# Kernel tuning notes

Measured on AMD Instinct MI355X. Metric: run time of the kernel, lower is better.

## Reference

```python
import jax, jax.numpy as jnp
import numpy as np

B, N, E = 64, 1024, 16384  # graphs, nodes per graph, edges per graph
N_ITER = 5
NORMALIZE = True
NUM_INIT_LABELS = 16


def _unique_inverse(h):
    """Equivalent of torch.unique(h, sorted=True, return_inverse=True)[1] for 1-D h."""
    order = jnp.argsort(h)
    sh = h[order]
    bnd = jnp.concatenate([jnp.zeros(1, jnp.int32), (sh[1:] != sh[:-1]).astype(jnp.int32)])
    ranks = jnp.cumsum(bnd)  # dense rank in sorted-unique order
    return jnp.zeros_like(ranks).at[order].set(ranks)


def _wl_iteration(mask, labels, hash_w):
    """One WL iteration for all graphs.
    mask: [B,N,N] bool dense adjacency (sparse-to-dense, as in the torch code)
    labels: [B,N] int32
    hash_w: [2] float32 (Linear(2,1,bias=False) weight)
    Returns new labels [B,N] int32.
    """
    w0, w1 = hash_w[0], hash_w[1]
    lab_f = labels.astype(jnp.float32)
    deg = mask.sum(-1).astype(jnp.float32)                      # [B,N] valid-neighbor count
    K = deg.max(axis=-1, keepdims=True)                         # per-graph max_neighbors
    # sum of neighbor labels (gather+reduce over the dense mask, memory-bound)
    seg = jnp.einsum('bij,bj->bi', mask.astype(jnp.float32), lab_f)  # [B,N]
    # torch builds [N,max_neighbors] rows: node label in col 0-feature, sorted
    # neighbor labels (padded with -1) in col 1-feature, hashes each pair with
    # w0*node + w1*neigh and sums over columns. Closed form (sort is sum-invariant):
    #   K*w0*node + w1*(sum_neighbors - (K - deg))
    hashed = K * w0 * lab_f + w1 * (seg + deg - K)              # [B,N]
    return jax.vmap(_unique_inverse)(hashed)


def setup_inputs() -> dict:
    key = jax.random.key(0)
    k1, k2, k3, k4 = jax.random.split(key, 4)
    edge_src = jax.random.randint(k1, (B, E), 0, N, dtype=jnp.int32)
    edge_dst = jax.random.randint(k2, (B, E), 0, N, dtype=jnp.int32)
    labels = jax.random.randint(k3, (B, N), 0, NUM_INIT_LABELS, dtype=jnp.int32)
    hash_w = jax.random.normal(k4, (2,), dtype=jnp.float32)
    return {"edge_src": edge_src, "edge_dst": edge_dst, "labels": labels, "hash_w": hash_w}


def reference(edge_src, edge_dst, labels, hash_w):
    # sparse-to-dense neighbor mask, as in the torch module
    b_idx = jnp.arange(B, dtype=jnp.int32)[:, None]
    mask = jnp.zeros((B, N, N), dtype=bool).at[b_idx, edge_src, edge_dst].set(True)

    all_labels = [labels]
    for _ in range(N_ITER):
        all_labels.append(_wl_iteration(mask, all_labels[-1], hash_w))

    # feature vectors: per graph, bincount of labels summed over all iterations.
    # Labels are always < N (unique-inverse ranks < N; initial labels < 16),
    # so N bins is a tight static upper bound for torch's max_label+1; the extra
    # zero columns do not change the Gram matrix.
    labels_all = jnp.stack(all_labels, axis=1).reshape(B, -1)   # [B, (n_iter+1)*N]
    feats = jax.vmap(lambda l: jnp.zeros((N,), jnp.float32).at[l].add(1.0))(labels_all)

    kernel = feats @ feats.T                                    # [B,B]
    if NORMALIZE:
        d = jnp.sqrt(jnp.diag(kernel))
        kernel = kernel / (d[None, :] * d[:, None])
    return kernel
```

## Files before the change

### kernel.cpp

```cpp
#include <hip/hip_runtime.h>

#define B 64
#define N 1024
#define E 16384
#define WPR 32
#define NITER 5
#define CSR_SLOTS (E + N)
#define MAXP 20

#define FEATS_OFF 0
#define DIAG_OFF  ((size_t)B * N * 4)

__global__ void __launch_bounds__(1024) wl_mega_k(const int* __restrict__ src,
                                                  const int* __restrict__ dstp,
                                                  const int* __restrict__ lab0,
                                                  const float* __restrict__ hw,
                                                  unsigned int* __restrict__ feats,
                                                  float* __restrict__ diag) {
    __shared__ union {
        unsigned int chunk[N * WPR];
        struct {
            unsigned short nbr[CSR_SLOTS];
            struct {
                int hist[N];
                int scan[N];
                float grp[N];
                int flag[N];
            } pb;
            int meta[N];
            unsigned short perm[N];
            int dh[256];
            int dtop[256];
        } s;
    } u;
    __shared__ int s_lab[N + 2];
    __shared__ unsigned int s_feats[N];
    __shared__ int s_wsum[16];
    __shared__ int s_kp[16];
    __shared__ float s_mn[16], s_mx[16];
    __shared__ float s_gmn, s_gmx;
    __shared__ int s_K;
    __shared__ int s_anytie;
    int b = blockIdx.x, t = threadIdx.x;
    int lane = t & 63, w = t >> 6;

#pragma unroll
    for (int k = 0; k < 8; ++k)
        ((uint4*)u.chunk)[t + k * 1024] = make_uint4(0, 0, 0, 0);
    int l0 = lab0[(size_t)b * N + t];
    s_lab[t] = l0;
    s_feats[t] = 0;
    if (t == 0) { s_lab[N] = 0; s_anytie = 0; }
    __syncthreads();
#pragma unroll
    for (int v = 0; v < 16; ++v) {
        unsigned long long m = __ballot(l0 == v);
        if (lane == v) {
            int c = __popcll(m);
            if (c) atomicAdd(&s_feats[v], (unsigned)c);
        }
    }

    const int* sg = src + (size_t)b * E;
    const int* dg_ = dstp + (size_t)b * E;
#pragma unroll
    for (int k = 0; k < 16; ++k) {
        int es = sg[t + k * 1024];
        int ed = dg_[t + k * 1024];
        int wlog = ed >> 5;
        int g = wlog >> 2;
        int p = (g + es) & 7;
        atomicOr(&u.chunk[es * WPR + p * 4 + (wlog & 3)], 1u << (ed & 31));
    }
    __syncthreads();
    uint4 r[8];
    {
        const uint4* row4 = (const uint4*)(u.chunk + t * WPR);
#pragma unroll
        for (int g = 0; g < 8; ++g)
            r[g] = row4[(g + t) & 7];
    }
    __syncthreads();

    int dg = 0;
#pragma unroll
    for (int k = 0; k < 8; ++k)
        dg += __popc(r[k].x) + __popc(r[k].y) + __popc(r[k].z) + __popc(r[k].w);
    int alloc = (dg + 1) & ~1;

    int f = alloc;
#pragma unroll
    for (int d2 = 1; d2 < 64; d2 <<= 1) {
        int v = __shfl_up(f, d2);
        if (lane >= d2) f += v;
    }
    int km = dg;
#pragma unroll
    for (int o = 32; o > 0; o >>= 1) km = max(km, __shfl_down(km, o));
    if (lane == 63) s_wsum[w] = f;
    if (lane == 0)  s_kp[w] = km;
    __syncthreads();
    if (w == 0) {
        int orig = (lane < 16) ? s_wsum[lane] : 0;
        int v = orig;
#pragma unroll
        for (int d2 = 1; d2 < 16; d2 <<= 1) {
            int uu = __shfl_up(v, d2);
            if (lane >= d2) v += uu;
        }
        if (lane < 16) s_wsum[lane] = v - orig;
        int kk = (lane < 16) ? s_kp[lane] : 0;
#pragma unroll
        for (int m2 = 8; m2 >= 1; m2 >>= 1) kk = max(kk, __shfl_xor(kk, m2));
        if (lane == 0) s_K = kk;
    }
    __syncthreads();
    int start = (f - alloc) + s_wsum[w];
    u.s.pb.hist[t] = 0;
    u.s.pb.flag[t] = 0;
    if (t < 256) u.s.dh[t] = 0;

    {
        int idx = start;
#pragma unroll
        for (int k = 0; k < 8; ++k) {
            unsigned int wv[4] = { r[k].x, r[k].y, r[k].z, r[k].w };
#pragma unroll
            for (int c2 = 0; c2 < 4; ++c2) {
                unsigned int word = wv[c2];
                int bb = (k * 4 + c2) << 5;
                while (word) {
                    int j = __ffs(word) - 1;
                    word &= word - 1;
                    u.s.nbr[idx++] = (unsigned short)(bb + j);
                }
            }
        }
        if (dg & 1) u.s.nbr[idx] = (unsigned short)N;
    }
    u.s.meta[t] = (start << 11) | dg;
    float Kf = (float)s_K;
    float w0 = hw[0], w1 = hw[1];
    __syncthreads();

    atomicAdd(&u.s.dh[min(dg, 255)], 1);
    __syncthreads();
    if (w == 0) {
        int h0 = u.s.dh[lane * 4], h1 = u.s.dh[lane * 4 + 1];
        int h2 = u.s.dh[lane * 4 + 2], h3 = u.s.dh[lane * 4 + 3];
        int c1 = h0 + h1, c2 = c1 + h2, c3 = c2 + h3;
        int ex = c3;
#pragma unroll
        for (int d2 = 1; d2 < 64; d2 <<= 1) {
            int v = __shfl_up(ex, d2);
            if (lane >= d2) ex += v;
        }
        ex -= c3;
        u.s.dtop[lane * 4]     = N - (ex + h0);
        u.s.dtop[lane * 4 + 1] = N - (ex + c1);
        u.s.dtop[lane * 4 + 2] = N - (ex + c2);
        u.s.dtop[lane * 4 + 3] = N - (ex + c3);
    }
    __syncthreads();
    {
        int pos = atomicAdd(&u.s.dtop[min(dg, 255)], 1);
        u.s.perm[pos] = (unsigned short)t;
    }
    __syncthreads();
    int v_node = u.s.perm[t];
    int mv = u.s.meta[v_node];
    int vdeg = mv & 2047;
    int vpstart = (mv >> 11) >> 1;
    int vpairs = ((vdeg + 1) & ~1) >> 1;
    int lab_reg = s_lab[v_node];
    const unsigned int* nbr32 = (const unsigned int*)u.s.nbr;
    unsigned int pw[MAXP];
#pragma unroll
    for (int k = 0; k < MAXP; ++k) {
        unsigned int pk = 0u;
        if (k < vpairs) pk = nbr32[vpstart + k];
        pw[k] = pk;
    }

    for (int it = 0; it < NITER; ++it) {
        int ssum = 0;
#pragma unroll
        for (int k = 0; k < MAXP; ++k) if (k < vpairs) {
            unsigned int pr = pw[k];
            ssum += s_lab[pr & 0xFFFFu] + s_lab[pr >> 16];
        }
        for (int k = MAXP; k < vpairs; ++k) {
            unsigned int pr = nbr32[vpstart + k];
            ssum += s_lab[pr & 0xFFFFu] + s_lab[pr >> 16];
        }
        float t1 = __fmul_rn(__fmul_rn(Kf, w0), (float)lab_reg);
        float t2 = __fmul_rn(w1, __fsub_rn(__fadd_rn((float)ssum, (float)vdeg), Kf));
        float h  = __fadd_rn(t1, t2);

        float mn = h, mx = h;
#pragma unroll
        for (int o = 32; o > 0; o >>= 1) {
            mn = fminf(mn, __shfl_down(mn, o));
            mx = fmaxf(mx, __shfl_down(mx, o));
        }
        if (lane == 0) { s_mn[w] = mn; s_mx[w] = mx; }
        __syncthreads();
        if (w == 0) {
            float a = (lane < 16) ? s_mn[lane] : 3.4e38f;
            float c = (lane < 16) ? s_mx[lane] : -3.4e38f;
#pragma unroll
            for (int m2 = 8; m2 >= 1; m2 >>= 1) {
                a = fminf(a, __shfl_xor(a, m2));
                c = fmaxf(c, __shfl_xor(c, m2));
            }
            if (lane == 0) { s_gmn = a; s_gmx = c; }
        }
        __syncthreads();
        float fmn = s_gmn;
        float span = s_gmx - fmn;
        float scale = (span > 0.f) ? (1023.0f / span) : 0.f;
        int bucket = min((int)((h - fmn) * scale), 1023);
        int off_in = atomicAdd(&u.s.pb.hist[bucket], 1);
        __syncthreads();

        f = u.s.pb.hist[t];
#pragma unroll
        for (int d2 = 1; d2 < 64; d2 <<= 1) {
            int v = __shfl_up(f, d2);
            if (lane >= d2) f += v;
        }
        if (lane == 63) s_wsum[w] = f;
        __syncthreads();
        if (w == 0) {
            int orig = (lane < 16) ? s_wsum[lane] : 0;
            int v = orig;
#pragma unroll
            for (int d2 = 1; d2 < 16; d2 <<= 1) {
                int uu = __shfl_up(v, d2);
                if (lane >= d2) v += uu;
            }
            if (lane < 16) s_wsum[lane] = v - orig;
        }
        __syncthreads();
        u.s.pb.scan[t] = f + s_wsum[w];
        __syncthreads();

        int bs = u.s.pb.scan[bucket] - u.s.pb.hist[bucket];
        int be = u.s.pb.scan[bucket];
        u.s.pb.grp[bs + off_in] = h;
        __syncthreads();

        int c = bs;
        int eq = 0;
        for (int k = bs; k < be; ++k) {
            float g = u.s.pb.grp[k];
            c += (g < h);
            eq += (g == h);
        }
        if (eq > 1) s_anytie = it + 1;
        u.s.pb.hist[t] = 0;
        __syncthreads();

        int rank;
        if (s_anytie != it + 1) {
            rank = c;
            s_lab[v_node] = rank;
            lab_reg = rank;
            s_feats[rank] += 1u;
        } else {
            u.s.pb.flag[c] = 1;
            __syncthreads();
            int f2 = u.s.pb.flag[t];
#pragma unroll
            for (int d2 = 1; d2 < 64; d2 <<= 1) {
                int v = __shfl_up(f2, d2);
                if (lane >= d2) f2 += v;
            }
            if (lane == 63) s_wsum[w] = f2;
            __syncthreads();
            if (w == 0) {
                int orig = (lane < 16) ? s_wsum[lane] : 0;
                int v = orig;
#pragma unroll
                for (int d2 = 1; d2 < 16; d2 <<= 1) {
                    int uu = __shfl_up(v, d2);
                    if (lane >= d2) v += uu;
                }
                if (lane < 16) s_wsum[lane] = v - orig;
            }
            __syncthreads();
            u.s.pb.scan[t] = f2 + s_wsum[w];
            u.s.pb.flag[t] = 0;
            __syncthreads();
            rank = u.s.pb.scan[c] - 1;
            s_lab[v_node] = rank;
            lab_reg = rank;
            atomicAdd(&s_feats[rank], 1u);
        }
        __syncthreads();
    }

    unsigned int fv = s_feats[t];
    feats[(size_t)b * N + t] = fv;
    int sq = (int)(fv * fv);
#pragma unroll
    for (int o = 32; o > 0; o >>= 1) sq += __shfl_down(sq, o);
    if (lane == 0) s_wsum[w] = sq;
    __syncthreads();
    if (t == 0) {
        int tot = 0;
#pragma unroll
        for (int k = 0; k < 16; ++k) tot += s_wsum[k];
        diag[b] = (float)tot;
    }
}

__global__ void __launch_bounds__(256) gram_k(const unsigned int* __restrict__ feats,
                                              const float* __restrict__ diag,
                                              float* __restrict__ out) {
    __shared__ unsigned int s_fi[N];
    int i = blockIdx.x, t = threadIdx.x;
    int lane = t & 63, w = t >> 6;
    ((uint4*)s_fi)[t] = ((const uint4*)(feats + (size_t)i * N))[t];
    __syncthreads();
    float di = diag[i];
    for (int jj = 0; jj < 16; ++jj) {
        int j = w * 16 + jj;
        const uint4* fj = (const uint4*)(feats + (size_t)j * N);
        const uint4* fi = (const uint4*)s_fi;
        int s = 0;
#pragma unroll
        for (int k = 0; k < 4; ++k) {
            uint4 vb = fj[lane + k * 64];
            uint4 va = fi[lane + k * 64];
            s += (int)(va.x * vb.x) + (int)(va.y * vb.y)
               + (int)(va.z * vb.z) + (int)(va.w * vb.w);
        }
#pragma unroll
        for (int off = 32; off > 0; off >>= 1) s += __shfl_down(s, off);
        if (lane == 0) out[i * B + j] = (float)s / sqrtf(di * diag[j]);
    }
}

extern "C" void kernel_launch(void* const* d_in, const int* in_sizes, int n_in,
                              void* d_out, int out_size, void* d_ws, size_t ws_size,
                              hipStream_t stream) {
    const int*   esrc = (const int*)d_in[0];
    const int*   edst = (const int*)d_in[1];
    const int*   lab0 = (const int*)d_in[2];
    const float* hw   = (const float*)d_in[3];

    char* ws = (char*)d_ws;
    unsigned int* feats = (unsigned int*)(ws + FEATS_OFF);
    float*        diag  = (float*)(ws + DIAG_OFF);

    wl_mega_k<<<B, 1024, 0, stream>>>(esrc, edst, lab0, hw, feats, diag);
    gram_k<<<B, 256, 0, stream>>>(feats, diag, (float*)d_out);
}
```

Baseline: 110.5 us.

## Drop block barriers via redundant per-wave reductions and defer fast-path histogram

Every wave now redundantly computes the cross-wave min/max, the scan offsets and the max degree from shared partials with xor shuffles. This replaces the wave-0 reduction plus an extra __syncthreads in setup and in each WL iteration. The edge and label global loads are hoisted to the top of the kernel so their latency overlaps shared-memory zeroing. In the tie-free path the ranks form a permutation, so each bin's count increment is replaced by a per-thread counter added once at the end. The cost is a few redundant shuffles and LDS reads per wave, plus more live registers for the preloaded edges.

```diff
diff --git a/kernel.cpp b/kernel.cpp
--- a/kernel.cpp
+++ b/kernel.cpp
@@ -38,16 +38,23 @@
     __shared__ int s_wsum[16];
     __shared__ int s_kp[16];
     __shared__ float s_mn[16], s_mx[16];
-    __shared__ float s_gmn, s_gmx;
-    __shared__ int s_K;
     __shared__ int s_anytie;
     int b = blockIdx.x, t = threadIdx.x;
     int lane = t & 63, w = t >> 6;
 
+    const int* sg = src + (size_t)b * E;
+    const int* dg_ = dstp + (size_t)b * E;
+    int es[16], ed[16];
+#pragma unroll
+    for (int k = 0; k < 16; ++k) {
+        es[k] = sg[t + k * 1024];
+        ed[k] = dg_[t + k * 1024];
+    }
+    int l0 = lab0[(size_t)b * N + t];
+    float w0 = hw[0], w1 = hw[1];
 #pragma unroll
     for (int k = 0; k < 8; ++k)
         ((uint4*)u.chunk)[t + k * 1024] = make_uint4(0, 0, 0, 0);
-    int l0 = lab0[(size_t)b * N + t];
     s_lab[t] = l0;
     s_feats[t] = 0;
     if (t == 0) { s_lab[N] = 0; s_anytie = 0; }
@@ -61,16 +68,12 @@
         }
     }
 
-    const int* sg = src + (size_t)b * E;
-    const int* dg_ = dstp + (size_t)b * E;
 #pragma unroll
     for (int k = 0; k < 16; ++k) {
-        int es = sg[t + k * 1024];
-        int ed = dg_[t + k * 1024];
-        int wlog = ed >> 5;
+        int wlog = ed[k] >> 5;
         int g = wlog >> 2;
-        int p = (g + es) & 7;
-        atomicOr(&u.chunk[es * WPR + p * 4 + (wlog & 3)], 1u << (ed & 31));
+        int p = (g + es[k]) & 7;
+        atomicOr(&u.chunk[es[k] * WPR + p * 4 + (wlog & 3)], 1u << (ed[k] & 31));
     }
     __syncthreads();
     uint4 r[8];
@@ -100,22 +103,18 @@
     if (lane == 63) s_wsum[w] = f;
     if (lane == 0)  s_kp[w] = km;
     __syncthreads();
-    if (w == 0) {
-        int orig = (lane < 16) ? s_wsum[lane] : 0;
-        int v = orig;
-#pragma unroll
-        for (int d2 = 1; d2 < 16; d2 <<= 1) {
-            int uu = __shfl_up(v, d2);
-            if (lane >= d2) v += uu;
-        }
-        if (lane < 16) s_wsum[lane] = v - orig;
-        int kk = (lane < 16) ? s_kp[lane] : 0;
+    float Kf;
+    int start;
+    {
+        int vv = ((lane & 15) < w) ? s_wsum[lane & 15] : 0;
+#pragma unroll
+        for (int m2 = 1; m2 < 16; m2 <<= 1) vv += __shfl_xor(vv, m2);
+        start = (f - alloc) + vv;
+        int kk = s_kp[lane & 15];
 #pragma unroll
         for (int m2 = 8; m2 >= 1; m2 >>= 1) kk = max(kk, __shfl_xor(kk, m2));
-        if (lane == 0) s_K = kk;
-    }
-    __syncthreads();
-    int start = (f - alloc) + s_wsum[w];
+        Kf = (float)kk;
+    }
     u.s.pb.hist[t] = 0;
     u.s.pb.flag[t] = 0;
     if (t < 256) u.s.dh[t] = 0;
@@ -139,8 +138,6 @@
         if (dg & 1) u.s.nbr[idx] = (unsigned short)N;
     }
     u.s.meta[t] = (start << 11) | dg;
-    float Kf = (float)s_K;
-    float w0 = hw[0], w1 = hw[1];
     __syncthreads();
 
     atomicAdd(&u.s.dh[min(dg, 255)], 1);
@@ -182,6 +179,7 @@
         pw[k] = pk;
     }
 
+    int nfast = 0;
     for (int it = 0; it < NITER; ++it) {
         int ssum = 0;
 #pragma unroll
@@ -205,19 +203,18 @@
         }
         if (lane == 0) { s_mn[w] = mn; s_mx[w] = mx; }
         __syncthreads();
-        if (w == 0) {
-            float a = (lane < 16) ? s_mn[lane] : 3.4e38f;
-            float c = (lane < 16) ? s_mx[lane] : -3.4e38f;
+        float fmn, span;
+        {
+            float a = s_mn[lane & 15];
+            float cmx = s_mx[lane & 15];
 #pragma unroll
             for (int m2 = 8; m2 >= 1; m2 >>= 1) {
                 a = fminf(a, __shfl_xor(a, m2));
-                c = fmaxf(c, __shfl_xor(c, m2));
+                cmx = fmaxf(cmx, __shfl_xor(cmx, m2));
             }
-            if (lane == 0) { s_gmn = a; s_gmx = c; }
-        }
-        __syncthreads();
-        float fmn = s_gmn;
-        float span = s_gmx - fmn;
+            fmn = a;
+            span = cmx - a;
+        }
         float scale = (span > 0.f) ? (1023.0f / span) : 0.f;
         int bucket = min((int)((h - fmn) * scale), 1023);
         int off_in = atomicAdd(&u.s.pb.hist[bucket], 1);
@@ -231,18 +228,12 @@
         }
         if (lane == 63) s_wsum[w] = f;
         __syncthreads();
-        if (w == 0) {
-            int orig = (lane < 16) ? s_wsum[lane] : 0;
-            int v = orig;
-#pragma unroll
-            for (int d2 = 1; d2 < 16; d2 <<= 1) {
-                int uu = __shfl_up(v, d2);
-                if (lane >= d2) v += uu;
-            }
-            if (lane < 16) s_wsum[lane] = v - orig;
-        }
-        __syncthreads();
-        u.s.pb.scan[t] = f + s_wsum[w];
+        {
+            int vv = ((lane & 15) < w) ? s_wsum[lane & 15] : 0;
+#pragma unroll
+            for (int m2 = 1; m2 < 16; m2 <<= 1) vv += __shfl_xor(vv, m2);
+            u.s.pb.scan[t] = f + vv;
+        }
         __syncthreads();
 
         int bs = u.s.pb.scan[bucket] - u.s.pb.hist[bucket];
@@ -250,25 +241,23 @@
         u.s.pb.grp[bs + off_in] = h;
         __syncthreads();
 
-        int c = bs;
+        int cr = bs;
         int eq = 0;
         for (int k = bs; k < be; ++k) {
             float g = u.s.pb.grp[k];
-            c += (g < h);
+            cr += (g < h);
             eq += (g == h);
         }
         if (eq > 1) s_anytie = it + 1;
         u.s.pb.hist[t] = 0;
         __syncthreads();
 
-        int rank;
         if (s_anytie != it + 1) {
-            rank = c;
-            s_lab[v_node] = rank;
-            lab_reg = rank;
-            s_feats[rank] += 1u;
+            s_lab[v_node] = cr;
+            lab_reg = cr;
+            ++nfast;
         } else {
-            u.s.pb.flag[c] = 1;
+            u.s.pb.flag[cr] = 1;
             __syncthreads();
             int f2 = u.s.pb.flag[t];
 #pragma unroll
@@ -278,21 +267,15 @@
             }
             if (lane == 63) s_wsum[w] = f2;
             __syncthreads();
-            if (w == 0) {
-                int orig = (lane < 16) ? s_wsum[lane] : 0;
-                int v = orig;
-#pragma unroll
-                for (int d2 = 1; d2 < 16; d2 <<= 1) {
-                    int uu = __shfl_up(v, d2);
-                    if (lane >= d2) v += uu;
-                }
-                if (lane < 16) s_wsum[lane] = v - orig;
+            {
+                int vv = ((lane & 15) < w) ? s_wsum[lane & 15] : 0;
+#pragma unroll
+                for (int m2 = 1; m2 < 16; m2 <<= 1) vv += __shfl_xor(vv, m2);
+                u.s.pb.scan[t] = f2 + vv;
             }
-            __syncthreads();
-            u.s.pb.scan[t] = f2 + s_wsum[w];
             u.s.pb.flag[t] = 0;
             __syncthreads();
-            rank = u.s.pb.scan[c] - 1;
+            int rank = u.s.pb.scan[cr] - 1;
             s_lab[v_node] = rank;
             lab_reg = rank;
             atomicAdd(&s_feats[rank], 1u);
@@ -300,7 +283,7 @@
         __syncthreads();
     }
 
-    unsigned int fv = s_feats[t];
+    unsigned int fv = s_feats[t] + (unsigned)nfast;
     feats[(size_t)b * N + t] = fv;
     int sq = (int)(fv * fv);
 #pragma unroll
```

Result: faster. 104.9 us (-5.0%).
